# Kernel optimization log

Hardware: AMD Instinct MI355X
Metric: run time of the kernel (lower is better)

## Reference

```python
import jax, jax.numpy as jnp
import numpy as np

N_FREQS = 6  # PositionEmbedding N_freqs when embedding=='pe'

def _pe(x):
    freqs = (2.0 ** jnp.arange(N_FREQS)).astype(x.dtype)
    fx = x * freqs  # [B,Q,N_FREQS]
    sc = jnp.stack([jnp.sin(fx), jnp.cos(fx)], axis=-1).reshape(fx.shape[0], fx.shape[1], 2 * N_FREQS)
    return jnp.concatenate([x, sc], axis=-1)

def _mlp(h, W1, b1, W2, b2, W3, b3):
    h = jax.nn.relu(h @ W1 + b1)
    h = jax.nn.relu(h @ W2 + b2)
    return h @ W3 + b3

def setup_inputs() -> dict:
    key = jax.random.key(0)
    B, Q, N, D, H = 4, 65536, 8192, 16, 128
    ks = jax.random.split(key, 6)
    coord = jax.random.uniform(ks[0], (B, Q, 1), minval=-1.0, maxval=1.0, dtype=jnp.float32)
    latent = jax.random.normal(ks[1], (B, N, D), dtype=jnp.float32)
    in_dim = (1 + 2 * N_FREQS) + 3 * D  # pe(rel_coord) ++ unfolded feat = 13 + 48 = 61
    def init(k, shp, fan):
        return (jax.random.normal(k, shp, dtype=jnp.float32) / np.float32(np.sqrt(fan)))
    W1 = init(ks[2], (in_dim, H), in_dim); b1 = jnp.zeros((H,), jnp.float32)
    W2 = init(ks[3], (H, H), H);          b2 = jnp.zeros((H,), jnp.float32)
    W3 = init(ks[4], (H, 1), H);          b3 = jnp.zeros((1,), jnp.float32)
    return dict(coord=coord, latent=latent, W1=W1, b1=b1, W2=W2, b2=b2, W3=W3, b3=b3)

def reference(coord, latent, W1, b1, W2, b2, W3, b3):
    B, Q, _ = coord.shape
    N = latent.shape[1]
    # feat_unfold: concat shifted-prev / self / shifted-next along feature dim -> [B,N,3D]
    prev = jnp.concatenate([latent[:, :1], latent[:, :-1]], axis=1)
    nxt = jnp.concatenate([latent[:, 1:], latent[:, -1:]], axis=1)
    feat = jnp.concatenate([prev, latent, nxt], axis=-1)
    # make_coord grid: cell centers in [-1,1]
    grid = (-1.0 + (2.0 * jnp.arange(N, dtype=coord.dtype) + 1.0) / N)
    rx = 1.0 / N           # 2/num_latents/2
    eps_shift = 1e-6
    preds, areas = [], []
    for vx in (-2.0, 0.0):  # eval path vx_lst
        c = jnp.clip(coord + vx * rx + eps_shift, -1.0 + 1e-6, 1.0 - 1e-6)
        idx = jnp.clip(jnp.searchsorted(grid, c[..., 0]), 0, N - 1)  # [B,Q]
        q_coord = grid[idx][..., None]                               # [B,Q,1]
        q_feat = jnp.take_along_axis(feat, idx[..., None], axis=1)   # [B,Q,3D]
        rel = (coord - q_coord) * N                                  # scaled rel coord
        area = jnp.abs(rel[..., 0]) + 1e-9                           # [B,Q]
        inp = jnp.concatenate([_pe(rel), q_feat], axis=-1)           # [B,Q,61]
        preds.append(_mlp(inp, W1, b1, W2, b2, W3, b3))              # [B,Q,1]
        areas.append(area)
    tot = areas[0] + areas[1]
    # local_ensemble: swap areas before weighting
    ret = preds[0] * (areas[1] / tot)[..., None] + preds[1] * (areas[0] / tot)[..., None]
    return ret
```

## Files before the change

kernel.cpp:

```cpp
#include <hip/hip_runtime.h>
#include <hip/hip_bf16.h>

typedef short s8v __attribute__((ext_vector_type(8)));
typedef float f4v __attribute__((ext_vector_type(4)));
typedef unsigned u4v __attribute__((ext_vector_type(4)));

__device__ __forceinline__ unsigned short f2bf(float x) {
  unsigned u = __builtin_bit_cast(unsigned, x);
  u += 0x7fffu + ((u >> 16) & 1u);
  return (unsigned short)(u >> 16);
}
#if __has_builtin(__builtin_amdgcn_cvt_pk_bf16_f32)
__device__ __forceinline__ unsigned pk2(float a, float b) {
  return __builtin_bit_cast(unsigned, __builtin_amdgcn_cvt_pk_bf16_f32(a, b));
}
#else
__device__ __forceinline__ unsigned pk2(float a, float b) {
  unsigned ua = __builtin_bit_cast(unsigned, a) + 0x8000u;
  unsigned ub = __builtin_bit_cast(unsigned, b) + 0x8000u;
  return __builtin_amdgcn_perm(ub, ua, 0x07060302u);
}
#endif

__device__ __forceinline__ void g2lds16(const void* g, void* l) {
  __builtin_amdgcn_global_load_lds(
      (const __attribute__((address_space(1))) unsigned*)g,
      (__attribute__((address_space(3))) unsigned*)l, 16, 0, 0);
}

__global__ void prep_kernel(const float* __restrict__ W1, const float* __restrict__ b1,
                            const float* __restrict__ W2, const float* __restrict__ latent,
                            unsigned short* __restrict__ wsW) {
  int e = blockIdx.x * 256 + threadIdx.x;
  if (e < 8192) {
    int frag = e >> 9, rem = e & 511, lane = rem >> 3, j = rem & 7;
    int h = frag >> 1, ks = frag & 1;
    int q4 = lane >> 4, l15 = lane & 15;
    int k = ks * 32 + q4 * 8 + j;
    int n = h * 16 + l15;
    float v;
    if (k < 13) v = W1[k * 128 + n];
    else if (k == 13) v = b1[n];
    else if (k < 16) v = 0.0f;
    else v = W1[(k - 3) * 128 + n];
    wsW[e] = f2bf(v);
  } else if (e < 24576) {
    int e2 = e - 8192;
    int frag = e2 >> 9, rem = e2 & 511, lane = rem >> 3, j = rem & 7;
    int h2 = frag >> 2, ks = frag & 3;
    int q4 = lane >> 4, l15 = lane & 15;
    int kd = (j < 4) ? (32 * ks + 4 * q4 + j) : (32 * ks + 16 + 4 * q4 + (j - 4));
    int n = h2 * 16 + l15;
    wsW[e] = f2bf(W2[kd * 128 + n]);
  } else {
    int i = e - 24576;
    wsW[e] = f2bf(latent[i]);
  }
}

__global__ __launch_bounds__(256, 2) void lisagon_main(
    const float* __restrict__ coord, const unsigned short* __restrict__ latbf,
    const unsigned short* __restrict__ W1f, const unsigned short* __restrict__ W2f,
    const float* __restrict__ b2, const float* __restrict__ W3,
    const float* __restrict__ b3, float* __restrict__ out) {
  __shared__ __align__(16) unsigned short A1[256 * 64];
  __shared__ __align__(16) unsigned short W2s[16384];
  __shared__ float AREA[256];

  const int t = threadIdx.x;
  const int lane = t & 63, wv = t >> 6;
  const int l15 = lane & 15, q4 = lane >> 4;

#pragma unroll
  for (int it = 0; it < 8; it++) {
    int off = (it * 4 + wv) * 1024;
    g2lds16((const char*)W2f + off + lane * 16, (char*)W2s + off);
  }

  {
    const int r = t;
    const int Rg = blockIdx.x * 256 + r;
    const int gq = Rg >> 1, p = Rg & 1;
    const float co = coord[gq];
    float c = (co + (p ? 0.0f : -0.000244140625f)) + 1e-6f;
    c = fminf(fmaxf(c, -1.0f + 1e-6f), 1.0f - 1e-6f);
    double u = ((double)c * 8192.0 + 8191.0) * 0.5;
    int idx = (int)ceil(u);
    idx = min(max(idx, 0), 8191);

    float qc = ((float)(2 * idx + 1) - 8192.0f) * (1.0f / 8192.0f);
    float rel = (co - qc) * 8192.0f;
    AREA[r] = fabsf(rel) + 1e-9f;

    uint4* A1v = (uint4*)A1;
    const uint4* latv = (const uint4*)(latbf + (size_t)(gq >> 16) * (8192 * 16));
    int rows3[3];
    rows3[0] = max(idx - 1, 0);
    rows3[1] = idx;
    rows3[2] = min(idx + 1, 8191);
    uint4 L0[3], L1[3];
#pragma unroll
    for (int s = 0; s < 3; s++) {
      L0[s] = latv[rows3[s] * 2 + 0];
      L1[s] = latv[rows3[s] * 2 + 1];
    }

    float v[16];
    v[0] = rel;
    float f = rel;
#pragma unroll
    for (int i = 0; i < 6; i++) {
      v[1 + 2 * i] = __sinf(f);
      v[2 + 2 * i] = __cosf(f);
      f = f + f;
    }
    v[13] = 1.0f;
    v[14] = 0.0f; v[15] = 0.0f;
#pragma unroll
    for (int ch = 0; ch < 2; ch++) {
      union { uint4 u4; unsigned us[4]; } pkv;
#pragma unroll
      for (int w = 0; w < 4; w++) pkv.us[w] = pk2(v[ch * 8 + 2 * w], v[ch * 8 + 2 * w + 1]);
      A1v[r * 8 + (ch ^ (r & 7))] = pkv.u4;
    }
#pragma unroll
    for (int s = 0; s < 3; s++) {
      int ch0 = 2 + 2 * s;
      A1v[r * 8 + (ch0 ^ (r & 7))]       = L0[s];
      A1v[r * 8 + ((ch0 + 1) ^ (r & 7))] = L1[s];
    }
  }
  __syncthreads();

  const s8v* W1fv = (const s8v*)W1f;
  const s8v* W2sv = (const s8v*)W2s;
  const s8v* A1s  = (const s8v*)A1;
  const int rbase = wv * 64;

  s8v Bf[2][4];
#pragma unroll
  for (int ks = 0; ks < 2; ks++)
#pragma unroll
    for (int rt = 0; rt < 4; rt++) {
      int row = rbase + rt * 16 + l15;
      Bf[ks][rt] = A1s[row * 8 + ((ks * 4 + q4) ^ (row & 7))];
    }

  u4v bbv[4][4];
#pragma unroll
  for (int h = 0; h < 8; h++) {
    f4v a[4];
#pragma unroll
    for (int rt = 0; rt < 4; rt++) a[rt] = (f4v){0.f, 0.f, 0.f, 0.f};
#pragma unroll
    for (int ks = 0; ks < 2; ks++) {
      s8v Af = W1fv[(h * 2 + ks) * 64 + lane];
#pragma unroll
      for (int rt = 0; rt < 4; rt++)
        a[rt] = __builtin_amdgcn_mfma_f32_16x16x32_bf16(Af, Bf[ks][rt], a[rt], 0, 0, 0);
    }
#pragma unroll
    for (int rt = 0; rt < 4; rt++) {
      bbv[rt][h >> 1][2 * (h & 1)]     = pk2(fmaxf(a[rt][0], 0.f), fmaxf(a[rt][1], 0.f));
      bbv[rt][h >> 1][2 * (h & 1) + 1] = pk2(fmaxf(a[rt][2], 0.f), fmaxf(a[rt][3], 0.f));
    }
  }

  float s[4] = {0.f, 0.f, 0.f, 0.f};
#pragma unroll
  for (int h2 = 0; h2 < 8; h2++) {
    f4v a2[4];
    f4v b2v = ((const f4v*)b2)[h2 * 4 + q4];
#pragma unroll
    for (int rt = 0; rt < 4; rt++) a2[rt] = b2v;
#pragma unroll
    for (int ks = 0; ks < 4; ks++) {
      s8v Af = W2sv[(h2 * 4 + ks) * 64 + lane];
#pragma unroll
      for (int rt = 0; rt < 4; rt++)
        a2[rt] = __builtin_amdgcn_mfma_f32_16x16x32_bf16(
            Af, __builtin_bit_cast(s8v, bbv[rt][ks]), a2[rt], 0, 0, 0);
    }
    float4 w3v = ((const float4*)W3)[h2 * 4 + q4];
#pragma unroll
    for (int rt = 0; rt < 4; rt++) {
      s[rt] += fmaxf(a2[rt][0], 0.f) * w3v.x;
      s[rt] += fmaxf(a2[rt][1], 0.f) * w3v.y;
      s[rt] += fmaxf(a2[rt][2], 0.f) * w3v.z;
      s[rt] += fmaxf(a2[rt][3], 0.f) * w3v.w;
    }
  }

  const float b3s = b3[0];
#pragma unroll
  for (int rt = 0; rt < 4; rt++) {
    float pred = s[rt];
    pred += __shfl_xor(pred, 16, 64);
    pred += __shfl_xor(pred, 32, 64);
    pred += b3s;
    float other = __shfl_xor(pred, 1, 64);
    if (q4 == 0 && (l15 & 1) == 0) {
      int row0 = rbase + rt * 16 + l15;
      float a0 = AREA[row0], a1 = AREA[row0 + 1];
      float tot = a0 + a1;
      out[(blockIdx.x * 256 + row0) >> 1] = pred * (a1 / tot) + other * (a0 / tot);
    }
  }
}

extern "C" void kernel_launch(void* const* d_in, const int* in_sizes, int n_in,
                              void* d_out, int out_size, void* d_ws, size_t ws_size,
                              hipStream_t stream) {
  const float* coord  = (const float*)d_in[0];
  const float* latent = (const float*)d_in[1];
  const float* W1 = (const float*)d_in[2];
  const float* b1 = (const float*)d_in[3];
  const float* W2 = (const float*)d_in[4];
  const float* b2 = (const float*)d_in[5];
  const float* W3 = (const float*)d_in[6];
  const float* b3 = (const float*)d_in[7];
  float* out = (float*)d_out;
  unsigned short* wsW = (unsigned short*)d_ws;

  prep_kernel<<<2144, 256, 0, stream>>>(W1, b1, W2, latent, wsW);
  lisagon_main<<<2048, 256, 0, stream>>>(coord, wsW + 24576, wsW, wsW + 8192,
                                         b2, W3, b3, out);
}
```

Measured before the change: 100.4 us.

## Make main kernel persistent over four row tiles with register prefetch of next tile

```diff
diff --git a/kernel.cpp b/kernel.cpp
--- a/kernel.cpp
+++ b/kernel.cpp
@@ -65,11 +65,11 @@
     const float* __restrict__ b3, float* __restrict__ out) {
   __shared__ __align__(16) unsigned short A1[256 * 64];
   __shared__ __align__(16) unsigned short W2s[16384];
-  __shared__ float AREA[256];
 
   const int t = threadIdx.x;
   const int lane = t & 63, wv = t >> 6;
   const int l15 = lane & 15, q4 = lane >> 4;
+  const int wgRow = blockIdx.x * 1024;
 
 #pragma unroll
   for (int it = 0; it < 8; it++) {
@@ -77,9 +77,11 @@
     g2lds16((const char*)W2f + off + lane * 16, (char*)W2s + off);
   }
 
-  {
-    const int r = t;
-    const int Rg = blockIdx.x * 256 + r;
+  uint4 pL0[3], pL1[3];
+  unsigned pPE[8];
+  float pArea;
+
+  auto do_prefetch = [&](int Rg) {
     const int gq = Rg >> 1, p = Rg & 1;
     const float co = coord[gq];
     float c = (co + (p ? 0.0f : -0.000244140625f)) + 1e-6f;
@@ -87,24 +89,14 @@
     double u = ((double)c * 8192.0 + 8191.0) * 0.5;
     int idx = (int)ceil(u);
     idx = min(max(idx, 0), 8191);
-
+    const uint4* latv = (const uint4*)latbf + (size_t)(gq >> 16) * 16384;
+    int r0 = max(idx - 1, 0), r2 = min(idx + 1, 8191);
+    pL0[0] = latv[r0 * 2];  pL1[0] = latv[r0 * 2 + 1];
+    pL0[1] = latv[idx * 2]; pL1[1] = latv[idx * 2 + 1];
+    pL0[2] = latv[r2 * 2];  pL1[2] = latv[r2 * 2 + 1];
     float qc = ((float)(2 * idx + 1) - 8192.0f) * (1.0f / 8192.0f);
     float rel = (co - qc) * 8192.0f;
-    AREA[r] = fabsf(rel) + 1e-9f;
-
-    uint4* A1v = (uint4*)A1;
-    const uint4* latv = (const uint4*)(latbf + (size_t)(gq >> 16) * (8192 * 16));
-    int rows3[3];
-    rows3[0] = max(idx - 1, 0);
-    rows3[1] = idx;
-    rows3[2] = min(idx + 1, 8191);
-    uint4 L0[3], L1[3];
-#pragma unroll
-    for (int s = 0; s < 3; s++) {
-      L0[s] = latv[rows3[s] * 2 + 0];
-      L1[s] = latv[rows3[s] * 2 + 1];
-    }
-
+    pArea = fabsf(rel) + 1e-9f;
     float v[16];
     v[0] = rel;
     float f = rel;
@@ -117,93 +109,107 @@
     v[13] = 1.0f;
     v[14] = 0.0f; v[15] = 0.0f;
 #pragma unroll
-    for (int ch = 0; ch < 2; ch++) {
-      union { uint4 u4; unsigned us[4]; } pkv;
-#pragma unroll
-      for (int w = 0; w < 4; w++) pkv.us[w] = pk2(v[ch * 8 + 2 * w], v[ch * 8 + 2 * w + 1]);
-      A1v[r * 8 + (ch ^ (r & 7))] = pkv.u4;
-    }
-#pragma unroll
-    for (int s = 0; s < 3; s++) {
-      int ch0 = 2 + 2 * s;
-      A1v[r * 8 + (ch0 ^ (r & 7))]       = L0[s];
-      A1v[r * 8 + ((ch0 + 1) ^ (r & 7))] = L1[s];
-    }
-  }
-  __syncthreads();
+    for (int w = 0; w < 8; w++) pPE[w] = pk2(v[2 * w], v[2 * w + 1]);
+  };
+
+  do_prefetch(wgRow + t);
 
   const s8v* W1fv = (const s8v*)W1f;
   const s8v* W2sv = (const s8v*)W2s;
   const s8v* A1s  = (const s8v*)A1;
   const int rbase = wv * 64;
-
-  s8v Bf[2][4];
-#pragma unroll
-  for (int ks = 0; ks < 2; ks++)
+  const float b3s = b3[0];
+
+  for (int tile = 0; tile < 4; tile++) {
+    const float myArea = pArea;
+    {
+      const int r = t;
+      uint4* A1v = (uint4*)A1;
+      uint4 q0, q1;
+      q0.x = pPE[0]; q0.y = pPE[1]; q0.z = pPE[2]; q0.w = pPE[3];
+      q1.x = pPE[4]; q1.y = pPE[5]; q1.z = pPE[6]; q1.w = pPE[7];
+      A1v[r * 8 + (0 ^ (r & 7))] = q0;
+      A1v[r * 8 + (1 ^ (r & 7))] = q1;
+#pragma unroll
+      for (int s = 0; s < 3; s++) {
+        int ch0 = 2 + 2 * s;
+        A1v[r * 8 + (ch0 ^ (r & 7))]       = pL0[s];
+        A1v[r * 8 + ((ch0 + 1) ^ (r & 7))] = pL1[s];
+      }
+    }
+    __syncthreads();
+
+    s8v Bf[2][4];
+#pragma unroll
+    for (int ks = 0; ks < 2; ks++)
+#pragma unroll
+      for (int rt = 0; rt < 4; rt++) {
+        int row = rbase + rt * 16 + l15;
+        Bf[ks][rt] = A1s[row * 8 + ((ks * 4 + q4) ^ (row & 7))];
+      }
+    __syncthreads();
+
+    if (tile + 1 < 4) do_prefetch(wgRow + (tile + 1) * 256 + t);
+
+    u4v bbv[4][4];
+#pragma unroll
+    for (int h = 0; h < 8; h++) {
+      f4v a[4];
+#pragma unroll
+      for (int rt = 0; rt < 4; rt++) a[rt] = (f4v){0.f, 0.f, 0.f, 0.f};
+#pragma unroll
+      for (int ks = 0; ks < 2; ks++) {
+        s8v Af = W1fv[(h * 2 + ks) * 64 + lane];
+#pragma unroll
+        for (int rt = 0; rt < 4; rt++)
+          a[rt] = __builtin_amdgcn_mfma_f32_16x16x32_bf16(Af, Bf[ks][rt], a[rt], 0, 0, 0);
+      }
+#pragma unroll
+      for (int rt = 0; rt < 4; rt++) {
+        bbv[rt][h >> 1][2 * (h & 1)]     = pk2(fmaxf(a[rt][0], 0.f), fmaxf(a[rt][1], 0.f));
+        bbv[rt][h >> 1][2 * (h & 1) + 1] = pk2(fmaxf(a[rt][2], 0.f), fmaxf(a[rt][3], 0.f));
+      }
+    }
+
+    float s[4] = {0.f, 0.f, 0.f, 0.f};
+#pragma unroll
+    for (int h2 = 0; h2 < 8; h2++) {
+      f4v a2[4];
+      f4v b2v = ((const f4v*)b2)[h2 * 4 + q4];
+#pragma unroll
+      for (int rt = 0; rt < 4; rt++) a2[rt] = b2v;
+#pragma unroll
+      for (int ks = 0; ks < 4; ks++) {
+        s8v Af = W2sv[(h2 * 4 + ks) * 64 + lane];
+#pragma unroll
+        for (int rt = 0; rt < 4; rt++)
+          a2[rt] = __builtin_amdgcn_mfma_f32_16x16x32_bf16(
+              Af, __builtin_bit_cast(s8v, bbv[rt][ks]), a2[rt], 0, 0, 0);
+      }
+      float4 w3v = ((const float4*)W3)[h2 * 4 + q4];
+#pragma unroll
+      for (int rt = 0; rt < 4; rt++) {
+        s[rt] += fmaxf(a2[rt][0], 0.f) * w3v.x;
+        s[rt] += fmaxf(a2[rt][1], 0.f) * w3v.y;
+        s[rt] += fmaxf(a2[rt][2], 0.f) * w3v.z;
+        s[rt] += fmaxf(a2[rt][3], 0.f) * w3v.w;
+      }
+    }
+
 #pragma unroll
     for (int rt = 0; rt < 4; rt++) {
-      int row = rbase + rt * 16 + l15;
-      Bf[ks][rt] = A1s[row * 8 + ((ks * 4 + q4) ^ (row & 7))];
-    }
-
-  u4v bbv[4][4];
-#pragma unroll
-  for (int h = 0; h < 8; h++) {
-    f4v a[4];
-#pragma unroll
-    for (int rt = 0; rt < 4; rt++) a[rt] = (f4v){0.f, 0.f, 0.f, 0.f};
-#pragma unroll
-    for (int ks = 0; ks < 2; ks++) {
-      s8v Af = W1fv[(h * 2 + ks) * 64 + lane];
-#pragma unroll
-      for (int rt = 0; rt < 4; rt++)
-        a[rt] = __builtin_amdgcn_mfma_f32_16x16x32_bf16(Af, Bf[ks][rt], a[rt], 0, 0, 0);
-    }
-#pragma unroll
-    for (int rt = 0; rt < 4; rt++) {
-      bbv[rt][h >> 1][2 * (h & 1)]     = pk2(fmaxf(a[rt][0], 0.f), fmaxf(a[rt][1], 0.f));
-      bbv[rt][h >> 1][2 * (h & 1) + 1] = pk2(fmaxf(a[rt][2], 0.f), fmaxf(a[rt][3], 0.f));
-    }
-  }
-
-  float s[4] = {0.f, 0.f, 0.f, 0.f};
-#pragma unroll
-  for (int h2 = 0; h2 < 8; h2++) {
-    f4v a2[4];
-    f4v b2v = ((const f4v*)b2)[h2 * 4 + q4];
-#pragma unroll
-    for (int rt = 0; rt < 4; rt++) a2[rt] = b2v;
-#pragma unroll
-    for (int ks = 0; ks < 4; ks++) {
-      s8v Af = W2sv[(h2 * 4 + ks) * 64 + lane];
-#pragma unroll
-      for (int rt = 0; rt < 4; rt++)
-        a2[rt] = __builtin_amdgcn_mfma_f32_16x16x32_bf16(
-            Af, __builtin_bit_cast(s8v, bbv[rt][ks]), a2[rt], 0, 0, 0);
-    }
-    float4 w3v = ((const float4*)W3)[h2 * 4 + q4];
-#pragma unroll
-    for (int rt = 0; rt < 4; rt++) {
-      s[rt] += fmaxf(a2[rt][0], 0.f) * w3v.x;
-      s[rt] += fmaxf(a2[rt][1], 0.f) * w3v.y;
-      s[rt] += fmaxf(a2[rt][2], 0.f) * w3v.z;
-      s[rt] += fmaxf(a2[rt][3], 0.f) * w3v.w;
-    }
-  }
-
-  const float b3s = b3[0];
-#pragma unroll
-  for (int rt = 0; rt < 4; rt++) {
-    float pred = s[rt];
-    pred += __shfl_xor(pred, 16, 64);
-    pred += __shfl_xor(pred, 32, 64);
-    pred += b3s;
-    float other = __shfl_xor(pred, 1, 64);
-    if (q4 == 0 && (l15 & 1) == 0) {
-      int row0 = rbase + rt * 16 + l15;
-      float a0 = AREA[row0], a1 = AREA[row0 + 1];
-      float tot = a0 + a1;
-      out[(blockIdx.x * 256 + row0) >> 1] = pred * (a1 / tot) + other * (a0 / tot);
+      float pred = s[rt];
+      pred += __shfl_xor(pred, 16, 64);
+      pred += __shfl_xor(pred, 32, 64);
+      pred += b3s;
+      float other = __shfl_xor(pred, 1, 64);
+      float a0 = __shfl(myArea, rt * 16 + l15, 64);
+      float a1 = __shfl(myArea, rt * 16 + l15 + 1, 64);
+      if (q4 == 0 && (l15 & 1) == 0) {
+        int row0 = rbase + rt * 16 + l15;
+        float tot = a0 + a1;
+        out[(wgRow + tile * 256 + row0) >> 1] = pred * (a1 / tot) + other * (a0 / tot);
+      }
     }
   }
 }
@@ -223,6 +229,6 @@
   unsigned short* wsW = (unsigned short*)d_ws;
 
   prep_kernel<<<2144, 256, 0, stream>>>(W1, b1, W2, latent, wsW);
-  lisagon_main<<<2048, 256, 0, stream>>>(coord, wsW + 24576, wsW, wsW + 8192,
-                                         b2, W3, b3, out);
-}
+  lisagon_main<<<512, 256, 0, stream>>>(coord, wsW + 24576, wsW, wsW + 8192,
+                                        b2, W3, b3, out);
+}
```

Result: slower. 156.9 us (+56.3%).
